# Kernel optimization log

Hardware: AMD Instinct MI355X
Metric: run time of the kernel (lower is better)

Reference implementation:

```python
import jax, jax.numpy as jnp
import numpy as np

EPS = 1e-5

def group_norm(x, w, b, groups):
    # x: (B, C, *spatial)
    B, C = x.shape[0], x.shape[1]
    sp = x.shape[2:]
    xg = x.reshape(B, groups, C // groups, -1)
    mu = xg.mean(axis=(2, 3), keepdims=True)
    var = xg.var(axis=(2, 3), keepdims=True)
    xg = (xg - mu) * jax.lax.rsqrt(var + EPS)
    x = xg.reshape(B, C, *sp)
    shape = (1, C) + (1,) * len(sp)
    return x * w.reshape(shape) + b.reshape(shape)

def conv3d(x, w, bias=None):
    out = jax.lax.conv_general_dilated(
        x, w, window_strides=(1, 1, 1), padding='SAME',
        dimension_numbers=('NCDHW', 'OIDHW', 'NCDHW'))
    if bias is not None:
        out = out + bias.reshape(1, -1, 1, 1, 1)
    return out

def conv2d(x, w):
    return jax.lax.conv_general_dilated(
        x, w, window_strides=(1, 1), padding='SAME',
        dimension_numbers=('NCHW', 'OIHW', 'NCHW'))

def setup_inputs() -> dict:
    key = jax.random.key(0)
    ks = jax.random.split(key, 8)
    B, C, H, W = 8, 128, 64, 128
    fL = jax.random.normal(ks[0], (B, C, H, W), jnp.float32)
    fR = jax.random.normal(ks[1], (B, C, H, W), jnp.float32)
    s = 0.05
    w1 = jax.random.normal(ks[2], (16, 8, 3, 3, 3), jnp.float32) * s
    w2 = jax.random.normal(ks[3], (16, 16, 3, 3, 3), jnp.float32) * s
    w3 = jax.random.normal(ks[4], (1, 16, 3, 3, 3), jnp.float32) * s
    b3 = jnp.zeros((1,), jnp.float32)
    gn1_w = jnp.ones((16,), jnp.float32); gn1_b = jnp.zeros((16,), jnp.float32)
    gn2_w = jnp.ones((16,), jnp.float32); gn2_b = jnp.zeros((16,), jnp.float32)
    fh_w = jax.random.normal(ks[5], (16, 128, 3, 3), jnp.float32) * s
    fh_gn_w = jnp.ones((16,), jnp.float32); fh_gn_b = jnp.zeros((16,), jnp.float32)
    return dict(fL=fL, fR=fR, w1=w1, gn1_w=gn1_w, gn1_b=gn1_b,
                w2=w2, gn2_w=gn2_w, gn2_b=gn2_b, w3=w3, b3=b3,
                fh_w=fh_w, fh_gn_w=fh_gn_w, fh_gn_b=fh_gn_b)

MAX_DISP = 24
GROUPS = 8

def reference(fL, fR, w1, gn1_w, gn1_b, w2, gn2_w, gn2_b, w3, b3,
              fh_w, fh_gn_w, fh_gn_b):
    B, C, H, W = fL.shape
    cg = C // GROUPS
    fL_g = fL.reshape(B, GROUPS, cg, H, W)
    cv_slices = []
    for d in range(MAX_DISP):  # small fixed loop over disparities
        fR_s = fR if d == 0 else jnp.pad(fR[:, :, :, :W - d], ((0, 0), (0, 0), (0, 0), (d, 0)))
        fR_g = fR_s.reshape(B, GROUPS, cg, H, W)
        cv_slices.append(jnp.mean(fL_g * fR_g, axis=2))  # (B, G, H, W)
    cv = jnp.stack(cv_slices, axis=2)  # (B, G, D, H, W)
    x = jax.nn.silu(group_norm(conv3d(cv, w1), gn1_w, gn1_b, 8))
    x = jax.nn.silu(group_norm(conv3d(x, w2), gn2_w, gn2_b, 8))
    logits = conv3d(x, w3, b3)[:, 0]  # (B, D, H, W)
    prob = jax.nn.softmax(logits, axis=1)
    disp_idx = jnp.arange(MAX_DISP, dtype=prob.dtype).reshape(1, MAX_DISP, 1, 1)
    d_out = jnp.sum(prob * disp_idx, axis=1, keepdims=True)  # (B,1,H,W)
    conf = jnp.max(prob, axis=1, keepdims=True)
    sx = jnp.zeros_like(d_out)
    sy = jnp.zeros_like(d_out)
    feat = jax.nn.silu(group_norm(conv2d(fL, fh_w), fh_gn_w, fh_gn_b, 8))
    return (d_out, sx, sy, feat, conf)
```

## Files before the change

kernel.cpp:

```cpp
#include <hip/hip_runtime.h>
#include <math.h>

#define B_   8
#define CIN  128
#define H_   64
#define W_   128
#define D_   24
#define HW_  (H_*W_)

typedef _Float16 half_t;
typedef __attribute__((ext_vector_type(8))) _Float16 half8;
typedef __attribute__((ext_vector_type(4))) _Float16 half4;
typedef __attribute__((ext_vector_type(4))) float f32x4;

#define CVB   0
#define X1B   25165824
#define X2B   75497472
#define STB   125829120
#define GN1_STATS 0
#define GN1_SS    128
#define GN2_STATS 384
#define GN2_SS    512
#define GN3_STATS 768
#define GN3_SS    896
#define ST_COUNT  1152
#define WQ1B  (STB + 16384)
#define WQ2B  (WQ1B + 7168)
#define WQFB  (WQ2B + 14336)

#define OUT_D    0
#define OUT_SX   65536
#define OUT_SY   131072
#define OUT_FEAT 196608
#define OUT_CONF 1245184

__global__ __launch_bounds__(256) void prepack_k(
    const float* __restrict__ w1, const float* __restrict__ w2,
    const float* __restrict__ fw, half_t* __restrict__ wq1,
    half_t* __restrict__ wq2, half_t* __restrict__ wqf2) {
  int i = blockIdx.x * 256 + threadIdx.x;
  if (i < 3584) {
    int s = i >> 9, l = (i >> 3) & 63, j = i & 7;
    int o = l & 15;
    int k = s * 32 + ((l >> 4) << 3) + j;
    float v = 0.f;
    if (k < 216) {
      int tap = k >> 3, c = k & 7;
      int kz = tap / 9, kyx = tap % 9;
      v = w1[((o * 8 + c) * 3 + kz) * 9 + kyx];
    }
    wq1[i] = (half_t)v;
  } else if (i < 3584 + 7168) {
    int ii = i - 3584;
    int s = ii >> 9, l = (ii >> 3) & 63, j = ii & 7;
    int o = l & 15;
    int k = s * 32 + ((l >> 4) << 3) + j;
    float v = 0.f;
    if (k < 432) {
      int tap = k >> 4, c = k & 15;
      int kz = tap / 9, kyx = tap % 9;
      v = w2[((o * 16 + c) * 3 + kz) * 9 + kyx];
    }
    wq2[ii] = (half_t)v;
  } else if (i < 3584 + 7168 + 18432) {
    int jj = i - (3584 + 7168);
    int cc = jj / 4608, rem = jj % 4608;
    int s = rem >> 9, l = (rem >> 3) & 63, j = rem & 7;
    int o = l & 15;
    int c = cc * 32 + ((l >> 4) << 3) + j;
    wqf2[jj] = (half_t)fw[(o * CIN + c) * 9 + s];
  }
}

__global__ __launch_bounds__(128) void cost_volume_k(
    const float* __restrict__ fL, const float* __restrict__ fR,
    half_t* __restrict__ cvt) {
  int w  = threadIdx.x;
  int d  = blockIdx.x % D_;
  int bh = blockIdx.x / D_;
  int h  = bh & 63;
  int b  = bh >> 6;

  float acc[8];
#pragma unroll
  for (int g = 0; g < 8; ++g) acc[g] = 0.f;

  int wr = w - d;
  if (wr >= 0) {
    const float* pL = fL + (size_t)b * CIN * HW_ + h * W_ + w;
    const float* pR = fR + (size_t)b * CIN * HW_ + h * W_ + wr;
#pragma unroll
    for (int g = 0; g < 8; ++g) {
      float a = 0.f;
#pragma unroll
      for (int ci = 0; ci < 16; ++ci) {
        int c = g * 16 + ci;
        a = fmaf(pL[(size_t)c * HW_], pR[(size_t)c * HW_], a);
      }
      acc[g] = a;
    }
  }
  size_t p = (((size_t)b * D_ + d) * H_ + h) * W_ + w;
  half8 ov;
#pragma unroll
  for (int g = 0; g < 8; ++g) ov[g] = (half_t)(acc[g] * 0.0625f);
  *(half8*)(cvt + p * 8) = ov;
}

template <int CI, bool NORM>
__global__ __launch_bounds__(256, 2) void conv_mfma_k(
    const half_t* __restrict__ in, const half_t* __restrict__ wq,
    half_t* __restrict__ outp, float* __restrict__ stats,
    const float* __restrict__ nss) {
  constexpr int KS    = (CI == 16) ? 14 : 7;
  constexpr int PITCH = (CI == 16) ? 24 : 8;
  constexpr int TPS   = 32 / CI;

  __shared__ half_t act[3 * 340 * PITCH];
  __shared__ float redS[4][16], redQ[4][16];

  int tid = threadIdx.x;
  int l = tid & 63, w = tid >> 6;
  int bid = blockIdx.x;
  int xt = bid & 3, yt = (bid >> 2) & 7;
  int r5 = bid >> 5;
  int zc = r5 % 3, b = r5 / 3;
  int z0 = zc * 8;
  int y0 = yt * 8, x0 = xt * 32;

  half8 wfrag[KS];
#pragma unroll
  for (int s = 0; s < KS; ++s)
    wfrag[s] = *(const half8*)(wq + (s * 64 + l) * 8);

  float sc[8], sh[8];
  if (NORM) {
    int c0 = (tid & 1) * 8;
#pragma unroll
    for (int j = 0; j < 8; ++j) {
      sc[j] = nss[b * 32 + (c0 + j) * 2];
      sh[j] = nss[b * 32 + (c0 + j) * 2 + 1];
    }
  }

  auto fill = [&](int zi, int slot) {
    if (CI == 16) {
      for (int u = tid; u < 680; u += 256) {
        int chunk = u & 1, pix = u >> 1;
        int yy = pix / 34, xx = pix - yy * 34;
        int gy = y0 - 1 + yy, gx = x0 - 1 + xx;
        half8 v = {0, 0, 0, 0, 0, 0, 0, 0};
        if ((unsigned)zi < 24u && (unsigned)gy < 64u && (unsigned)gx < 128u) {
          half8 rr = *(const half8*)(in +
              ((((size_t)b * D_ + zi) * H_ + gy) * W_ + gx) * 16 + chunk * 8);
          if (NORM) {
#pragma unroll
            for (int j = 0; j < 8; ++j) {
              float t = fmaf((float)rr[j], sc[j], sh[j]);
              v[j] = (half_t)(t / (1.f + __expf(-t)));
            }
          } else {
            v = rr;
          }
        }
        *(half8*)(act + (slot * 340 + pix) * PITCH + chunk * 8) = v;
      }
    } else {
      for (int u = tid; u < 340; u += 256) {
        int yy = u / 34, xx = u - yy * 34;
        int gy = y0 - 1 + yy, gx = x0 - 1 + xx;
        half8 v = {0, 0, 0, 0, 0, 0, 0, 0};
        if ((unsigned)zi < 24u && (unsigned)gy < 64u && (unsigned)gx < 128u)
          v = *(const half8*)(in +
              ((((size_t)b * D_ + zi) * H_ + gy) * W_ + gx) * 8);
        *(half8*)(act + (slot * 340 + u) * PITCH) = v;
      }
    }
  };

  int q = l >> 4, n = l & 15;
  int chalf  = (CI == 16) ? (q & 1) * 8 : 0;
  int tapadd = (CI == 16) ? (q >> 1) : q;
  int ntoff[4];
#pragma unroll
  for (int nt = 0; nt < 4; ++nt)
    ntoff[nt] = ((2 * w + (nt >> 1)) * 34 + (nt & 1) * 16) * PITCH;

  float sacc[4] = {0.f, 0.f, 0.f, 0.f}, qacc[4] = {0.f, 0.f, 0.f, 0.f};

  fill(z0 - 1, z0 % 3);
  fill(z0, (z0 + 1) % 3);

  for (int z = z0; z < z0 + 8; ++z) {
    fill(z + 1, (z + 2) % 3);
    __syncthreads();
    int zm3 = z % 3;

    f32x4 accv[4];
#pragma unroll
    for (int nt = 0; nt < 4; ++nt) accv[nt] = (f32x4){0.f, 0.f, 0.f, 0.f};

#pragma unroll
    for (int s = 0; s < KS; ++s) {
      int tap = TPS * s + tapadd;
      tap = tap > 26 ? 26 : tap;
      int kz = (tap * 57) >> 9;
      int t9 = tap - kz * 9;
      int ky = (t9 * 11) >> 5;
      int kx = t9 - ky * 3;
      int sl = zm3 + kz; if (sl >= 3) sl -= 3;
      int base = (sl * 340 + ky * 34 + kx + n) * PITCH + chalf;
#pragma unroll
      for (int nt = 0; nt < 4; ++nt) {
        half8 bf = *(const half8*)(act + base + ntoff[nt]);
        accv[nt] =
            __builtin_amdgcn_mfma_f32_16x16x32_f16(wfrag[s], bf, accv[nt], 0, 0, 0);
      }
    }

#pragma unroll
    for (int nt = 0; nt < 4; ++nt) {
      int ygl = y0 + 2 * w + (nt >> 1);
      int xgl = x0 + (nt & 1) * 16 + n;
      half4 o;
#pragma unroll
      for (int r = 0; r < 4; ++r) {
        float v = accv[nt][r];
        o[r] = (half_t)v;
        sacc[r] += v;
        qacc[r] = fmaf(v, v, qacc[r]);
      }
      *(half4*)(outp + ((((size_t)b * D_ + z) * H_ + ygl) * W_ + xgl) * 16 +
                q * 4) = o;
    }
    __syncthreads();
  }

#pragma unroll
  for (int r = 0; r < 4; ++r) {
#pragma unroll
    for (int m = 1; m < 16; m <<= 1) {
      sacc[r] += __shfl_xor(sacc[r], m);
      qacc[r] += __shfl_xor(qacc[r], m);
    }
  }
  if (n == 0) {
#pragma unroll
    for (int r = 0; r < 4; ++r) {
      redS[w][q * 4 + r] = sacc[r];
      redQ[w][q * 4 + r] = qacc[r];
    }
  }
  __syncthreads();
  if (tid < 16) {
    int g = tid >> 1;
    float v = 0.f;
    if (tid & 1) {
      for (int ww = 0; ww < 4; ++ww) v += redQ[ww][2 * g] + redQ[ww][2 * g + 1];
    } else {
      for (int ww = 0; ww < 4; ++ww) v += redS[ww][2 * g] + redS[ww][2 * g + 1];
    }
    atomicAdd(&stats[b * 16 + tid], v);
  }
}

__global__ __launch_bounds__(128) void gn_scale_k(
    const float* __restrict__ stats, const float* __restrict__ gw,
    const float* __restrict__ gb, float* __restrict__ ss, float inv_count) {
  int i = threadIdx.x;
  if (i < 128) {
    int c = i & 15, g = c >> 1, b = i >> 4;
    float sum = stats[(b * 8 + g) * 2];
    float sq  = stats[(b * 8 + g) * 2 + 1];
    float mean = sum * inv_count;
    float var  = sq * inv_count - mean * mean;
    float rstd = rsqrtf(var + 1e-5f);
    float scv = gw[c] * rstd;
    ss[i * 2] = scv;
    ss[i * 2 + 1] = gb[c] - mean * scv;
  }
}

__global__ __launch_bounds__(256) void conv3_softmax_k(
    const half_t* __restrict__ x2, const float* __restrict__ w3,
    const float* __restrict__ b3, const float* __restrict__ nss,
    float* __restrict__ out) {
  int xt = blockIdx.x & 3;
  int yt = (blockIdx.x >> 2) & 7;
  int b  = blockIdx.x >> 5;

  __shared__ float lg[26][256];
  __shared__ float plane[16 * 340];

  int tid = threadIdx.x;
  for (int r = 0; r < 26; ++r) lg[r][tid] = 0.f;

  float sc[8], sh[8];
  {
    int c0 = (tid & 1) * 8;
#pragma unroll
    for (int j = 0; j < 8; ++j) {
      sc[j] = nss[b * 32 + (c0 + j) * 2];
      sh[j] = nss[b * 32 + (c0 + j) * 2 + 1];
    }
  }

  int ty = tid >> 5, tx = tid & 31;
  int gy0 = yt * 8 - 1, gx0 = xt * 32 - 1;

  for (int zp = 0; zp < D_; ++zp) {
    __syncthreads();
    for (int u = tid; u < 680; u += 256) {
      int chunk = u & 1, pix = u >> 1;
      int yy = pix / 34, xx = pix - yy * 34;
      int gy = gy0 + yy, gx = gx0 + xx;
      int c0 = chunk * 8;
      if ((unsigned)gy < 64u && (unsigned)gx < 128u) {
        half8 rr = *(const half8*)(x2 +
            ((((size_t)b * D_ + zp) * H_ + gy) * W_ + gx) * 16 + c0);
#pragma unroll
        for (int j = 0; j < 8; ++j) {
          float t = fmaf((float)rr[j], sc[j], sh[j]);
          plane[(c0 + j) * 340 + pix] = t / (1.f + expf(-t));
        }
      } else {
#pragma unroll
        for (int j = 0; j < 8; ++j) plane[(c0 + j) * 340 + pix] = 0.f;
      }
    }
    __syncthreads();
    float pm = 0.f, p0 = 0.f, pp = 0.f;
#pragma unroll
    for (int c = 0; c < 16; ++c) {
#pragma unroll
      for (int ky = 0; ky < 3; ++ky) {
#pragma unroll
        for (int kx = 0; kx < 3; ++kx) {
          float v = plane[c * 340 + (ty + ky) * 34 + tx + kx];
          int wb = c * 27 + ky * 3 + kx;
          pm = fmaf(v, w3[wb + 18], pm);
          p0 = fmaf(v, w3[wb + 9],  p0);
          pp = fmaf(v, w3[wb],      pp);
        }
      }
    }
    lg[zp][tid]     += pm;
    lg[zp + 1][tid] += p0;
    lg[zp + 2][tid] += pp;
  }
  __syncthreads();

  float bias = b3[0];
  float lv[24], m = -1e30f;
#pragma unroll
  for (int z = 0; z < 24; ++z) {
    lv[z] = lg[z + 1][tid] + bias;
    m = fmaxf(m, lv[z]);
  }
  float s = 0.f, ds = 0.f;
#pragma unroll
  for (int z = 0; z < 24; ++z) {
    float e = expf(lv[z] - m);
    s += e;
    ds = fmaf(e, (float)z, ds);
  }
  float inv = 1.f / s;
  int y = yt * 8 + ty, x = xt * 32 + tx;
  out[OUT_D    + b * HW_ + y * W_ + x] = ds * inv;
  out[OUT_CONF + b * HW_ + y * W_ + x] = inv;
}

__global__ __launch_bounds__(256, 2) void feat_mfma_k(
    const float* __restrict__ fL, const half_t* __restrict__ wqf2,
    float* __restrict__ out, float* __restrict__ stats) {
  constexpr int PITCH = 40;

  __shared__ half_t act[340 * PITCH];
  __shared__ float redS[4][16], redQ[4][16];

  int tid = threadIdx.x;
  int l = tid & 63, w = tid >> 6;
  int xt = blockIdx.x & 3;
  int yt = (blockIdx.x >> 2) & 7;
  int b  = blockIdx.x >> 5;
  int y0 = yt * 8, x0 = xt * 32;

  int q = l >> 4, n = l & 15;
  int ntoff[4];
#pragma unroll
  for (int nt = 0; nt < 4; ++nt)
    ntoff[nt] = ((2 * w + (nt >> 1)) * 34 + (nt & 1) * 16) * PITCH;

  f32x4 accv[4];
#pragma unroll
  for (int nt = 0; nt < 4; ++nt) accv[nt] = (f32x4){0.f, 0.f, 0.f, 0.f};

  for (int cc = 0; cc < 4; ++cc) {
    half8 wfrag[9];
#pragma unroll
    for (int s = 0; s < 9; ++s)
      wfrag[s] = *(const half8*)(wqf2 + ((cc * 9 + s) * 64 + l) * 8);

    __syncthreads();
    for (int u = tid; u < 1360; u += 256) {
      int qq = u & 3, pix = u >> 2;
      int yy = pix / 34, xx = pix - yy * 34;
      int gy = y0 - 1 + yy, gx = x0 - 1 + xx;
      half8 v = {0, 0, 0, 0, 0, 0, 0, 0};
      if ((unsigned)gy < 64u && (unsigned)gx < 128u) {
        const float* src = fL + ((size_t)(b * CIN + cc * 32 + qq * 8)) * HW_ +
                           gy * W_ + gx;
#pragma unroll
        for (int j = 0; j < 8; ++j) v[j] = (half_t)src[(size_t)j * HW_];
      }
      *(half8*)(act + pix * PITCH + qq * 8) = v;
    }
    __syncthreads();

#pragma unroll
    for (int s = 0; s < 9; ++s) {
      int ky = s / 3, kx = s - ky * 3;
      int base = (ky * 34 + kx + n) * PITCH + q * 8;
#pragma unroll
      for (int nt = 0; nt < 4; ++nt) {
        half8 bf = *(const half8*)(act + base + ntoff[nt]);
        accv[nt] =
            __builtin_amdgcn_mfma_f32_16x16x32_f16(wfrag[s], bf, accv[nt], 0, 0, 0);
      }
    }
  }

  float sacc[4] = {0.f, 0.f, 0.f, 0.f}, qacc[4] = {0.f, 0.f, 0.f, 0.f};
#pragma unroll
  for (int nt = 0; nt < 4; ++nt) {
    int ygl = y0 + 2 * w + (nt >> 1);
    int xgl = x0 + (nt & 1) * 16 + n;
#pragma unroll
    for (int r = 0; r < 4; ++r) {
      float v = accv[nt][r];
      out[OUT_FEAT + (size_t)(b * 16 + q * 4 + r) * HW_ + ygl * W_ + xgl] = v;
      sacc[r] += v;
      qacc[r] = fmaf(v, v, qacc[r]);
    }
  }

#pragma unroll
  for (int r = 0; r < 4; ++r) {
#pragma unroll
    for (int m = 1; m < 16; m <<= 1) {
      sacc[r] += __shfl_xor(sacc[r], m);
      qacc[r] += __shfl_xor(qacc[r], m);
    }
  }
  if (n == 0) {
#pragma unroll
    for (int r = 0; r < 4; ++r) {
      redS[w][q * 4 + r] = sacc[r];
      redQ[w][q * 4 + r] = qacc[r];
    }
  }
  __syncthreads();
  if (tid < 16) {
    int g = tid >> 1;
    float v = 0.f;
    if (tid & 1) {
      for (int ww = 0; ww < 4; ++ww) v += redQ[ww][2 * g] + redQ[ww][2 * g + 1];
    } else {
      for (int ww = 0; ww < 4; ++ww) v += redS[ww][2 * g] + redS[ww][2 * g + 1];
    }
    atomicAdd(&stats[b * 16 + tid], v);
  }
}

__global__ __launch_bounds__(256) void feat_finish_k(
    float* __restrict__ out, const float* __restrict__ ss) {
  int bid = blockIdx.x, tid = threadIdx.x;
  if (bid < 1024) {
    int idx4 = bid * 256 + tid;
    int bc = idx4 / 2048;
    float scv = ss[bc * 2], shv = ss[bc * 2 + 1];
    float4* p = reinterpret_cast<float4*>(out + OUT_FEAT) + idx4;
    float4 v = *p;
    float t;
    t = fmaf(v.x, scv, shv); v.x = t / (1.f + expf(-t));
    t = fmaf(v.y, scv, shv); v.y = t / (1.f + expf(-t));
    t = fmaf(v.z, scv, shv); v.z = t / (1.f + expf(-t));
    t = fmaf(v.w, scv, shv); v.w = t / (1.f + expf(-t));
    *p = v;
  } else {
    int i = (bid - 1024) * 256 + tid;
    float4 z = make_float4(0.f, 0.f, 0.f, 0.f);
    reinterpret_cast<float4*>(out + OUT_SX)[i] = z;
  }
}

extern "C" void kernel_launch(void* const* d_in, const int* in_sizes, int n_in,
                              void* d_out, int out_size, void* d_ws, size_t ws_size,
                              hipStream_t stream) {
  const float* fL      = (const float*)d_in[0];
  const float* fR      = (const float*)d_in[1];
  const float* w1      = (const float*)d_in[2];
  const float* gn1_w   = (const float*)d_in[3];
  const float* gn1_b   = (const float*)d_in[4];
  const float* w2      = (const float*)d_in[5];
  const float* gn2_w   = (const float*)d_in[6];
  const float* gn2_b   = (const float*)d_in[7];
  const float* w3      = (const float*)d_in[8];
  const float* b3      = (const float*)d_in[9];
  const float* fh_w    = (const float*)d_in[10];
  const float* fh_gn_w = (const float*)d_in[11];
  const float* fh_gn_b = (const float*)d_in[12];
  float* out = (float*)d_out;
  char*  W   = (char*)d_ws;

  half_t* cvt  = (half_t*)(W + CVB);
  half_t* x1b  = (half_t*)(W + X1B);
  half_t* x2b  = (half_t*)(W + X2B);
  float*  stF  = (float*)(W + STB);
  half_t* wq1  = (half_t*)(W + WQ1B);
  half_t* wq2  = (half_t*)(W + WQ2B);
  half_t* wqf2 = (half_t*)(W + WQFB);

  hipMemsetAsync(stF, 0, ST_COUNT * sizeof(float), stream);

  prepack_k<<<114, 256, 0, stream>>>(w1, w2, fh_w, wq1, wq2, wqf2);

  cost_volume_k<<<B_ * H_ * D_, 128, 0, stream>>>(fL, fR, cvt);

  conv_mfma_k<8, false><<<768, 256, 0, stream>>>(
      cvt, wq1, x1b, stF + GN1_STATS, nullptr);
  gn_scale_k<<<1, 128, 0, stream>>>(stF + GN1_STATS, gn1_w, gn1_b,
                                    stF + GN1_SS, 1.f / 393216.f);

  conv_mfma_k<16, true><<<768, 256, 0, stream>>>(
      x1b, wq2, x2b, stF + GN2_STATS, stF + GN1_SS);
  gn_scale_k<<<1, 128, 0, stream>>>(stF + GN2_STATS, gn2_w, gn2_b,
                                    stF + GN2_SS, 1.f / 393216.f);

  conv3_softmax_k<<<B_ * 8 * 4, 256, 0, stream>>>(x2b, w3, b3,
                                                  stF + GN2_SS, out);

  feat_mfma_k<<<B_ * 8 * 4, 256, 0, stream>>>(fL, wqf2, out, stF + GN3_STATS);
  gn_scale_k<<<1, 128, 0, stream>>>(stF + GN3_STATS, fh_gn_w, fh_gn_b,
                                    stF + GN3_SS, 1.f / 16384.f);
  feat_finish_k<<<1152, 256, 0, stream>>>(out, stF + GN3_SS);
}
```

Baseline: 437.1 us.

## Rework conv3+softmax with fp16 dot2, double-buffered planes and channel-split waves

Rewrites the final 3D conv plus softmax kernel. The SiLU'd input plane is now stored in shared memory as fp16 in a channel-interleaved layout, and the conv uses packed fp16 dot2 instructions against weights prepacked into a new buffer. Planes are double-buffered, so loading the next depth slice overlaps compute on the current one. Blocks grow to 512 threads, with two wave halves each taking 8 channels and keeping the 24 logits in registers, then combining them through shared memory before the softmax. The constant bias is dropped, which is safe because softmax is shift-invariant. The trade-off is fp16 rounding of activations and weights, plus higher register use per thread.

```diff
diff --git a/kernel.cpp b/kernel.cpp
--- a/kernel.cpp
+++ b/kernel.cpp
@@ -11,7 +11,17 @@
 typedef _Float16 half_t;
 typedef __attribute__((ext_vector_type(8))) _Float16 half8;
 typedef __attribute__((ext_vector_type(4))) _Float16 half4;
+typedef __attribute__((ext_vector_type(2))) _Float16 half2v;
 typedef __attribute__((ext_vector_type(4))) float f32x4;
+
+#if defined(__has_builtin)
+#if __has_builtin(__builtin_amdgcn_fdot2)
+#define FDOT2(a, b, c) __builtin_amdgcn_fdot2((a), (b), (c), false)
+#endif
+#endif
+#ifndef FDOT2
+#define FDOT2(a, b, c) ((c) + (float)(a)[0] * (float)(b)[0] + (float)(a)[1] * (float)(b)[1])
+#endif
 
 #define CVB   0
 #define X1B   25165824
@@ -27,6 +37,7 @@
 #define WQ1B  (STB + 16384)
 #define WQ2B  (WQ1B + 7168)
 #define WQFB  (WQ2B + 14336)
+#define WC3B  (WQFB + 36864)
 
 #define OUT_D    0
 #define OUT_SX   65536
@@ -36,8 +47,9 @@
 
 __global__ __launch_bounds__(256) void prepack_k(
     const float* __restrict__ w1, const float* __restrict__ w2,
-    const float* __restrict__ fw, half_t* __restrict__ wq1,
-    half_t* __restrict__ wq2, half_t* __restrict__ wqf2) {
+    const float* __restrict__ fw, const float* __restrict__ w3,
+    half_t* __restrict__ wq1, half_t* __restrict__ wq2,
+    half_t* __restrict__ wqf2, half_t* __restrict__ wc3) {
   int i = blockIdx.x * 256 + threadIdx.x;
   if (i < 3584) {
     int s = i >> 9, l = (i >> 3) & 63, j = i & 7;
@@ -69,6 +81,11 @@
     int o = l & 15;
     int c = cc * 32 + ((l >> 4) << 3) + j;
     wqf2[jj] = (half_t)fw[(o * CIN + c) * 9 + s];
+  } else if (i < 3584 + 7168 + 18432 + 432) {
+    int jj = i - (3584 + 7168 + 18432);
+    int c = jj & 15, tk = jj >> 4;
+    int kz = tk % 3, tap = tk / 3;
+    wc3[jj] = (half_t)w3[c * 27 + kz * 9 + tap];
   }
 }
 
@@ -281,19 +298,19 @@
   }
 }
 
-__global__ __launch_bounds__(256) void conv3_softmax_k(
-    const half_t* __restrict__ x2, const float* __restrict__ w3,
-    const float* __restrict__ b3, const float* __restrict__ nss,
-    float* __restrict__ out) {
+__global__ __launch_bounds__(512) void conv3_softmax_k(
+    const half_t* __restrict__ x2, const half_t* __restrict__ wc3,
+    const float* __restrict__ nss, float* __restrict__ out) {
+  constexpr int PITCH = 40;
+  __shared__ char pool[2 * 340 * PITCH * 2];
+  half_t* plane = (half_t*)pool;
+  float* part = (float*)pool;
+
+  int tid = threadIdx.x;
   int xt = blockIdx.x & 3;
   int yt = (blockIdx.x >> 2) & 7;
   int b  = blockIdx.x >> 5;
-
-  __shared__ float lg[26][256];
-  __shared__ float plane[16 * 340];
-
-  int tid = threadIdx.x;
-  for (int r = 0; r < 26; ++r) lg[r][tid] = 0.f;
+  int y0 = yt * 8, x0 = xt * 32;
 
   float sc[8], sh[8];
   {
@@ -305,69 +322,88 @@
     }
   }
 
-  int ty = tid >> 5, tx = tid & 31;
-  int gy0 = yt * 8 - 1, gx0 = xt * 32 - 1;
-
+  int wv = tid >> 6;
+  int ch = (wv >= 4) ? 8 : 0;
+  int pix = tid & 255;
+  int py = pix >> 5, px = pix & 31;
+  const uint* wu = (const uint*)wc3;
+
+  auto fill = [&](int zf, int buf) {
+    for (int u = tid; u < 680; u += 512) {
+      int chunk = u & 1, p = u >> 1;
+      int yy = p / 34, xx = p - yy * 34;
+      int gy = y0 - 1 + yy, gx = x0 - 1 + xx;
+      half8 v = {0, 0, 0, 0, 0, 0, 0, 0};
+      if ((unsigned)gy < 64u && (unsigned)gx < 128u) {
+        half8 rr = *(const half8*)(x2 +
+            ((((size_t)b * D_ + zf) * H_ + gy) * W_ + gx) * 16 + chunk * 8);
+#pragma unroll
+        for (int j = 0; j < 8; ++j) {
+          float t = fmaf((float)rr[j], sc[j], sh[j]);
+          v[j] = (half_t)(t / (1.f + __expf(-t)));
+        }
+      }
+      *(half8*)(plane + (buf * 340 + p) * PITCH + chunk * 8) = v;
+    }
+  };
+
+  float l[26];
+#pragma unroll
+  for (int z = 0; z < 26; ++z) l[z] = 0.f;
+
+  fill(0, 0);
+
+#pragma unroll
   for (int zp = 0; zp < D_; ++zp) {
     __syncthreads();
-    for (int u = tid; u < 680; u += 256) {
-      int chunk = u & 1, pix = u >> 1;
-      int yy = pix / 34, xx = pix - yy * 34;
-      int gy = gy0 + yy, gx = gx0 + xx;
-      int c0 = chunk * 8;
-      if ((unsigned)gy < 64u && (unsigned)gx < 128u) {
-        half8 rr = *(const half8*)(x2 +
-            ((((size_t)b * D_ + zp) * H_ + gy) * W_ + gx) * 16 + c0);
-#pragma unroll
-        for (int j = 0; j < 8; ++j) {
-          float t = fmaf((float)rr[j], sc[j], sh[j]);
-          plane[(c0 + j) * 340 + pix] = t / (1.f + expf(-t));
-        }
-      } else {
-#pragma unroll
-        for (int j = 0; j < 8; ++j) plane[(c0 + j) * 340 + pix] = 0.f;
-      }
-    }
-    __syncthreads();
-    float pm = 0.f, p0 = 0.f, pp = 0.f;
-#pragma unroll
-    for (int c = 0; c < 16; ++c) {
-#pragma unroll
-      for (int ky = 0; ky < 3; ++ky) {
-#pragma unroll
-        for (int kx = 0; kx < 3; ++kx) {
-          float v = plane[c * 340 + (ty + ky) * 34 + tx + kx];
-          int wb = c * 27 + ky * 3 + kx;
-          pm = fmaf(v, w3[wb + 18], pm);
-          p0 = fmaf(v, w3[wb + 9],  p0);
-          pp = fmaf(v, w3[wb],      pp);
-        }
-      }
-    }
-    lg[zp][tid]     += pm;
-    lg[zp + 1][tid] += p0;
-    lg[zp + 2][tid] += pp;
-  }
+    if (zp < D_ - 1) fill(zp + 1, (zp + 1) & 1);
+    const half_t* pb = plane + ((zp & 1) * 340) * PITCH + ch;
+#pragma unroll
+    for (int tap = 0; tap < 9; ++tap) {
+      int ky = tap / 3, kx = tap - ky * 3;
+      half8 av = *(const half8*)(pb + ((py + ky) * 34 + px + kx) * PITCH);
+      half2v pa0 = {av[0], av[1]}, pa1 = {av[2], av[3]};
+      half2v pa2 = {av[4], av[5]}, pa3 = {av[6], av[7]};
+#pragma unroll
+      for (int kz = 0; kz < 3; ++kz) {
+        const uint* wb = wu + (tap * 3 + kz) * 8 + (ch >> 1);
+        union { uint u; half2v h; } w0, w1, w2t, w3t;
+        w0.u = wb[0]; w1.u = wb[1]; w2t.u = wb[2]; w3t.u = wb[3];
+        float a = l[zp + 2 - kz];
+        a = FDOT2(pa0, w0.h, a);
+        a = FDOT2(pa1, w1.h, a);
+        a = FDOT2(pa2, w2t.h, a);
+        a = FDOT2(pa3, w3t.h, a);
+        l[zp + 2 - kz] = a;
+      }
+    }
+  }
+
   __syncthreads();
-
-  float bias = b3[0];
-  float lv[24], m = -1e30f;
-#pragma unroll
-  for (int z = 0; z < 24; ++z) {
-    lv[z] = lg[z + 1][tid] + bias;
-    m = fmaxf(m, lv[z]);
-  }
-  float s = 0.f, ds = 0.f;
-#pragma unroll
-  for (int z = 0; z < 24; ++z) {
-    float e = expf(lv[z] - m);
-    s += e;
-    ds = fmaf(e, (float)z, ds);
-  }
-  float inv = 1.f / s;
-  int y = yt * 8 + ty, x = xt * 32 + tx;
-  out[OUT_D    + b * HW_ + y * W_ + x] = ds * inv;
-  out[OUT_CONF + b * HW_ + y * W_ + x] = inv;
+  if (wv >= 4) {
+#pragma unroll
+    for (int z = 0; z < 24; ++z) part[pix * 25 + z] = l[z + 1];
+  }
+  __syncthreads();
+  if (wv < 4) {
+    float lv[24], m = -1e30f;
+#pragma unroll
+    for (int z = 0; z < 24; ++z) {
+      lv[z] = l[z + 1] + part[pix * 25 + z];
+      m = fmaxf(m, lv[z]);
+    }
+    float s = 0.f, ds = 0.f;
+#pragma unroll
+    for (int z = 0; z < 24; ++z) {
+      float e = __expf(lv[z] - m);
+      s += e;
+      ds = fmaf(e, (float)z, ds);
+    }
+    float inv = 1.f / s;
+    int y = y0 + py, x = x0 + px;
+    out[OUT_D    + b * HW_ + y * W_ + x] = ds * inv;
+    out[OUT_CONF + b * HW_ + y * W_ + x] = inv;
+  }
 }
 
 __global__ __launch_bounds__(256, 2) void feat_mfma_k(
@@ -506,7 +542,6 @@
   const float* gn2_w   = (const float*)d_in[6];
   const float* gn2_b   = (const float*)d_in[7];
   const float* w3      = (const float*)d_in[8];
-  const float* b3      = (const float*)d_in[9];
   const float* fh_w    = (const float*)d_in[10];
   const float* fh_gn_w = (const float*)d_in[11];
   const float* fh_gn_b = (const float*)d_in[12];
@@ -520,10 +555,11 @@
   half_t* wq1  = (half_t*)(W + WQ1B);
   half_t* wq2  = (half_t*)(W + WQ2B);
   half_t* wqf2 = (half_t*)(W + WQFB);
+  half_t* wc3  = (half_t*)(W + WC3B);
 
   hipMemsetAsync(stF, 0, ST_COUNT * sizeof(float), stream);
 
-  prepack_k<<<114, 256, 0, stream>>>(w1, w2, fh_w, wq1, wq2, wqf2);
+  prepack_k<<<116, 256, 0, stream>>>(w1, w2, fh_w, w3, wq1, wq2, wqf2, wc3);
 
   cost_volume_k<<<B_ * H_ * D_, 128, 0, stream>>>(fL, fR, cvt);
 
@@ -537,8 +573,7 @@
   gn_scale_k<<<1, 128, 0, stream>>>(stF + GN2_STATS, gn2_w, gn2_b,
                                     stF + GN2_SS, 1.f / 393216.f);
 
-  conv3_softmax_k<<<B_ * 8 * 4, 256, 0, stream>>>(x2b, w3, b3,
-                                                  stF + GN2_SS, out);
+  conv3_softmax_k<<<B_ * 8 * 4, 512, 0, stream>>>(x2b, wc3, stF + GN2_SS, out);
 
   feat_mfma_k<<<B_ * 8 * 4, 256, 0, stream>>>(fL, wqf2, out, stF + GN3_STATS);
   gn_scale_k<<<1, 128, 0, stream>>>(stF + GN3_STATS, fh_gn_w, fh_gn_b,
```

Result: no change. 430.4 us (-1.5%).
